# Optimization experiments

Hardware: AMD Instinct MI355X
Metric: run time of the kernel (lower is better)

## Reference

```python
import jax, jax.numpy as jnp
import numpy as np

B, S, D = 2, 2048, 1024
H, DK = 16, 64          # heads, d_k (= d_v)
DH = 4096               # FFN hidden
EPS = 1e-5


def _layer_norm(x, gamma, beta):
    mu = jnp.mean(x, axis=-1, keepdims=True)
    var = jnp.var(x, axis=-1, keepdims=True)
    return (x - mu) * jax.lax.rsqrt(var + EPS) * gamma + beta


def setup_inputs() -> dict:
    key = jax.random.key(0)
    ks = jax.random.split(key, 8)
    s = lambda fan_in: 1.0 / np.sqrt(fan_in)
    return {
        "x": jax.random.normal(ks[0], (B, S, D), dtype=jnp.float32),
        # NOTE: source module uses W_q for queries, keys AND values (bug kept faithfully),
        # so W_k / W_v are never used and are not materialized.
        "Wq": jax.random.normal(ks[1], (D, H * DK), dtype=jnp.float32) * s(D),
        "bq": jnp.zeros((H * DK,), dtype=jnp.float32),
        "Wo": jax.random.normal(ks[2], (H * DK, D), dtype=jnp.float32) * s(H * DK),
        "bo": jnp.zeros((D,), dtype=jnp.float32),
        "ln1_g": jnp.ones((D,), dtype=jnp.float32),
        "ln1_b": jnp.zeros((D,), dtype=jnp.float32),
        "W1": jax.random.normal(ks[3], (D, DH), dtype=jnp.float32) * s(D),
        "b1": jnp.zeros((DH,), dtype=jnp.float32),
        "W2": jax.random.normal(ks[4], (DH, D), dtype=jnp.float32) * s(DH),
        "b2": jnp.zeros((D,), dtype=jnp.float32),
        "ln2_g": jnp.ones((D,), dtype=jnp.float32),
        "ln2_b": jnp.zeros((D,), dtype=jnp.float32),
    }


def reference(x, Wq, bq, Wo, bo, ln1_g, ln1_b, W1, b1, W2, b2, ln2_g, ln2_b):
    residual = x
    # projections: q, k, v all use W_q (faithful to source)
    q = (x @ Wq + bq).reshape(B, S, H, DK)
    k = (x @ Wq + bq).reshape(B, S, H, DK)
    v = (x @ Wq + bq).reshape(B, S, H, DK)
    # scores scaled by sqrt(sequence_length), as in the source
    scale = 1.0 / jnp.sqrt(jnp.float32(S))
    scores = jnp.einsum("bqhd,bkhd->bhqk", q, k) * scale
    probs = jax.nn.softmax(scores, axis=-1)
    attn = jnp.einsum("bhqk,bkhd->bqhd", probs, v).reshape(B, S, H * DK)
    attn = attn @ Wo + bo
    # dropout is identity in eval mode
    x = _layer_norm(attn + residual, ln1_g, ln1_b)
    residual = x
    h = jax.nn.relu(x @ W1 + b1)
    x = h @ W2 + b2
    x = _layer_norm(x + residual, ln2_g, ln2_b)
    return x
```

## Files before the change

kernel.cpp:

```cpp
#include <hip/hip_runtime.h>
#include <stdint.h>


typedef unsigned short u16;
typedef __attribute__((ext_vector_type(8))) short v8s;
typedef __attribute__((ext_vector_type(4))) float v4f;

#define AS1 __attribute__((address_space(1)))
#define AS3 __attribute__((address_space(3)))

__device__ __forceinline__ void gl_lds16(const u16* g, u16* l) {
  __builtin_amdgcn_global_load_lds((const AS1 void*)g, (AS3 void*)l, 16, 0, 0);
}

__device__ __forceinline__ float bf2f(u16 u) {
  union { uint32_t i; float f; } v; v.i = ((uint32_t)u) << 16; return v.f;
}
__device__ __forceinline__ u16 f2bf(float f) {
  union { float f; uint32_t i; } v; v.f = f;
  uint32_t x = v.i;
  return (u16)((x + 0x7FFFu + ((x >> 16) & 1u)) >> 16);
}
__device__ __forceinline__ uint32_t fbits(float f) {
  union { float f; uint32_t u; } v; v.f = f; return v.u;
}

__global__ __launch_bounds__(256) void cvt_f2b(
    const float* __restrict__ src, u16* __restrict__ dst, int n4) {
  int i = (blockIdx.x * 256 + threadIdx.x);
  if (i < n4) {
    float4 v = *(const float4*)(src + (size_t)i * 4);
    ushort4 o;
    o.x = f2bf(v.x); o.y = f2bf(v.y); o.z = f2bf(v.z); o.w = f2bf(v.w);
    *(ushort4*)(dst + (size_t)i * 4) = o;
  }
}

__global__ __launch_bounds__(256) void transpose_f2b(
    const float* __restrict__ src, u16* __restrict__ dst,
    int R, int C, int ld_s, int ld_d) {
  __shared__ float tile[32][33];
  const int tx = threadIdx.x & 31, ty = threadIdx.x >> 5;
  const int c0 = blockIdx.x * 32, r0 = blockIdx.y * 32;
#pragma unroll
  for (int j = 0; j < 32; j += 8)
    tile[ty + j][tx] = src[(size_t)(r0 + ty + j) * ld_s + c0 + tx];
  __syncthreads();
#pragma unroll
  for (int j = 0; j < 32; j += 8)
    dst[(size_t)(c0 + ty + j) * ld_d + r0 + tx] = f2bf(tile[tx][ty + j]);
}

__global__ __launch_bounds__(256) void transpose_b2b(
    const u16* __restrict__ src, u16* __restrict__ dst,
    int R, int C, int ld_s, int ld_d) {
  __shared__ u16 tile[32][33];
  const int tx = threadIdx.x & 31, ty = threadIdx.x >> 5;
  const int c0 = blockIdx.x * 32, r0 = blockIdx.y * 32;
#pragma unroll
  for (int j = 0; j < 32; j += 8)
    tile[ty + j][tx] = src[(size_t)(r0 + ty + j) * ld_s + c0 + tx];
  __syncthreads();
#pragma unroll
  for (int j = 0; j < 32; j += 8)
    dst[(size_t)(c0 + ty + j) * ld_d + r0 + tx] = tile[tx][ty + j];
}

__global__ __launch_bounds__(512, 1) void gemm_8p(
    const u16* __restrict__ A, const u16* __restrict__ Bt,
    const float* __restrict__ bias, void* __restrict__ C0,
    u16* __restrict__ C1, u16* __restrict__ C2, u16* __restrict__ C3,
    int M, int N, int ldk, int klen, int relu, int c0_f32) {
  __shared__ u16 As[2][16384];
  __shared__ u16 Bs[2][16384];
  const int tid = threadIdx.x;
  const int w = tid >> 6, l = tid & 63;
  const int l16 = l & 15, kgrp = (l >> 4) & 3;
  const int wm = w >> 2, wn = w & 3;
  const int m0 = blockIdx.y * 256, n0 = blockIdx.x * 256;
  const int z = blockIdx.z;
  const int NT = klen >> 6;

  const int rl = tid >> 3;
  const int sw = 8 * ((tid & 7) ^ (rl & 7));
  const u16* gA[4]; const u16* gB[4];
#pragma unroll
  for (int j = 0; j < 4; j++) {
    gA[j] = A + (size_t)(m0 + j * 64 + rl) * ldk + (size_t)z * klen + sw;
    gB[j] = Bt + (size_t)(n0 + j * 64 + rl) * ldk + (size_t)z * klen + sw;
  }
  const int sdst = w * 512;

  const int ch0 = 8 * ((kgrp) ^ (l16 & 7));
  const int ch1 = 8 * ((4 + kgrp) ^ (l16 & 7));
  const int abase = (wm * 128 + l16) * 64;
  const int bbase = (wn * 64 + l16) * 64;

  v4f acc[8][4];
#pragma unroll
  for (int i = 0; i < 8; i++)
#pragma unroll
    for (int j = 0; j < 4; j++)
#pragma unroll
      for (int r = 0; r < 4; r++) acc[i][j][r] = 0.f;

  v8s a[4][2], b[4][2];

#define FENCE() asm volatile("" ::: "memory")
#define VMC(n) asm volatile("s_waitcnt vmcnt(" #n ")" ::: "memory")
#define BARX() { __builtin_amdgcn_s_barrier(); \
                 __builtin_amdgcn_sched_barrier(0); FENCE(); }
#define STGA(q, j, kt) gl_lds16(gA[j] + (size_t)(kt) * 64, &As[q][(j) * 4096 + sdst])
#define STGB(q, j, kt) gl_lds16(gB[j] + (size_t)(kt) * 64, &Bs[q][(j) * 4096 + sdst])
#define LDA(p, mh) { \
  const u16* Ap = &As[p][abase + (mh) * 4096]; \
  _Pragma("unroll") for (int mi = 0; mi < 4; mi++) { \
    a[mi][0] = *(const v8s*)(Ap + mi * 1024 + ch0); \
    a[mi][1] = *(const v8s*)(Ap + mi * 1024 + ch1); } }
#define LDB(p, nh) { \
  const u16* Bp = &Bs[p][bbase + (nh) * 2048]; \
  _Pragma("unroll") for (int ni = 0; ni < 2; ni++) { \
    b[(nh) * 2 + ni][0] = *(const v8s*)(Bp + ni * 1024 + ch0); \
    b[(nh) * 2 + ni][1] = *(const v8s*)(Bp + ni * 1024 + ch1); } }
#define MFQ(mh, nh) { \
  __builtin_amdgcn_s_setprio(1); \
  _Pragma("unroll") for (int ks = 0; ks < 2; ks++) \
  _Pragma("unroll") for (int mi = 0; mi < 4; mi++) \
  _Pragma("unroll") for (int ni = 0; ni < 2; ni++) \
    acc[(mh) * 4 + mi][(nh) * 2 + ni] = __builtin_amdgcn_mfma_f32_16x16x32_bf16( \
        a[mi][ks], b[(nh) * 2 + ni][ks], acc[(mh) * 4 + mi][(nh) * 2 + ni], 0, 0, 0); \
  __builtin_amdgcn_s_setprio(0); }

  STGA(0, 0, 0); STGA(0, 2, 0);
  FENCE();
  STGB(0, 0, 0); STGB(0, 1, 0);
  FENCE();
  STGB(0, 2, 0); STGB(0, 3, 0);
  FENCE();
  STGA(0, 1, 0); STGA(0, 3, 0);
  VMC(2); BARX();

  int p = 0;
  for (int kt = 0; kt < NT - 1; ++kt, p ^= 1) {
    const int q = p ^ 1;
    const int kn = kt + 1;
    LDA(p, 0);
    LDB(p, 0);
    FENCE();
    STGA(q, 0, kn); STGA(q, 2, kn);
    MFQ(0, 0);
    LDB(p, 1);
    FENCE();
    STGB(q, 0, kn); STGB(q, 1, kn);
    VMC(4); BARX();
    MFQ(0, 1);
    LDA(p, 1);
    FENCE();
    STGB(q, 2, kn); STGB(q, 3, kn);
    MFQ(1, 1);
    FENCE();
    STGA(q, 1, kn); STGA(q, 3, kn);
    VMC(2); BARX();
    MFQ(1, 0);
  }
  VMC(0); BARX();
  LDA(p, 0);
  LDB(p, 0);
  MFQ(0, 0);
  LDB(p, 1);
  MFQ(0, 1);
  LDA(p, 1);
  MFQ(1, 1);
  MFQ(1, 0);

#undef FENCE
#undef VMC
#undef BARX
#undef STGA
#undef STGB
#undef LDA
#undef LDB
#undef MFQ

#pragma unroll
  for (int mi = 0; mi < 8; mi++) {
    const int row = m0 + wm * 128 + mi * 16 + kgrp * 4;
#pragma unroll
    for (int ni = 0; ni < 4; ni++) {
      const int col = n0 + wn * 64 + ni * 16 + l16;
      float bv = (bias && z == 0) ? bias[col] : 0.f;
#pragma unroll
      for (int r = 0; r < 4; r++) {
        float v = acc[mi][ni][r] + bv;
        if (z == 0 && relu) v = fmaxf(v, 0.f);
        size_t idx = (size_t)(row + r) * N + col;
        if (z == 0) {
          if (c0_f32) ((float*)C0)[idx] = v;
          else ((u16*)C0)[idx] = f2bf(v);
        } else if (z == 1) {
          C1[idx] = f2bf(v);
        } else if (z == 2) {
          C2[idx] = f2bf(v);
        } else {
          C3[idx] = f2bf(v);
        }
      }
    }
  }
}

__global__ __launch_bounds__(256) void gemm_g2(
    const u16* __restrict__ A, const u16* __restrict__ Bt,
    const float* __restrict__ bias, void* __restrict__ C,
    int M, int N, int K, int relu, int accum, int out_f32) {
  __shared__ u16 As[2][8192];
  __shared__ u16 Bs[2][4096];
  const int tid = threadIdx.x;
  const int w = tid >> 6, l = tid & 63;
  const int l16 = l & 15, kgrp = l >> 4;
  const int m0 = blockIdx.y * 128, n0 = blockIdx.x * 64;
  const int wr = (w >> 1) * 64, wc = (w & 1) * 32;

  const int srow = w * 8 + (l >> 3);
  const u16* gA[4];
#pragma unroll
  for (int i = 0; i < 4; i++) {
    int r = i * 32 + srow;
    gA[i] = A + (size_t)(m0 + r) * K + 8 * ((l & 7) ^ (r & 7));
  }
  const u16* gB[2];
#pragma unroll
  for (int i = 0; i < 2; i++) {
    int r = i * 32 + srow;
    gB[i] = Bt + (size_t)(n0 + r) * K + 8 * ((l & 7) ^ (r & 7));
  }

  v4f acc[4][2];
#pragma unroll
  for (int i = 0; i < 4; i++)
#pragma unroll
    for (int j = 0; j < 2; j++)
#pragma unroll
      for (int r = 0; r < 4; r++) acc[i][j][r] = 0.f;

#pragma unroll
  for (int i = 0; i < 4; i++) gl_lds16(gA[i], &As[0][(i * 256 + w * 64) * 8]);
#pragma unroll
  for (int i = 0; i < 2; i++) gl_lds16(gB[i], &Bs[0][(i * 256 + w * 64) * 8]);

  int cur = 0;
  for (int k0 = 0; k0 < K; k0 += 64) {
    __syncthreads();
    if (k0 + 64 < K) {
      int nxt = cur ^ 1;
#pragma unroll
      for (int i = 0; i < 4; i++)
        gl_lds16(gA[i] + k0 + 64, &As[nxt][(i * 256 + w * 64) * 8]);
#pragma unroll
      for (int i = 0; i < 2; i++)
        gl_lds16(gB[i] + k0 + 64, &Bs[nxt][(i * 256 + w * 64) * 8]);
    }
    v8s a[4][2], b[2][2];
#pragma unroll
    for (int ks = 0; ks < 2; ks++) {
      int ch = 8 * ((ks * 4 + kgrp) ^ (l16 & 7));
#pragma unroll
      for (int mi = 0; mi < 4; mi++)
        a[mi][ks] = *(const v8s*)(&As[cur][(wr + mi * 16 + l16) * 64 + ch]);
#pragma unroll
      for (int ni = 0; ni < 2; ni++)
        b[ni][ks] = *(const v8s*)(&Bs[cur][(wc + ni * 16 + l16) * 64 + ch]);
    }
#pragma unroll
    for (int ks = 0; ks < 2; ks++)
#pragma unroll
      for (int mi = 0; mi < 4; mi++)
#pragma unroll
        for (int ni = 0; ni < 2; ni++)
          acc[mi][ni] = __builtin_amdgcn_mfma_f32_16x16x32_bf16(a[mi][ks], b[ni][ks], acc[mi][ni], 0, 0, 0);
    cur ^= 1;
  }

#pragma unroll
  for (int ni = 0; ni < 2; ni++) {
    int col = n0 + wc + ni * 16 + l16;
    float bv = bias ? bias[col] : 0.f;
#pragma unroll
    for (int mi = 0; mi < 4; mi++) {
      int row = m0 + wr + mi * 16 + kgrp * 4;
#pragma unroll
      for (int r = 0; r < 4; r++) {
        float v = acc[mi][ni][r] + bv;
        if (relu) v = fmaxf(v, 0.f);
        size_t idx = (size_t)(row + r) * N + col;
        if (out_f32) {
          float* Cf = (float*)C;
          if (accum) v += Cf[idx];
          Cf[idx] = v;
        } else {
          ((u16*)C)[idx] = f2bf(v);
        }
      }
    }
  }
}

__global__ __launch_bounds__(256) void attn_kernel(
    const u16* __restrict__ Q, const u16* __restrict__ Qt,
    u16* __restrict__ O) {
  __shared__ u16 KV[2][8192];
  __shared__ __align__(16) u16 Ps[4][2304];
  const int tid = threadIdx.x;
  const int w = tid >> 6, l = tid & 63;
  const int l16 = l & 15, kgrp = l >> 4;
  const int bh = blockIdx.y, b = bh >> 4, h = bh & 15;
  const int q0 = blockIdx.x * 128;
  const size_t rowQ = (size_t)(b * 2048 + q0 + w * 32);
  const float cexp = 1.4426950408889634f / 45.254833995939045f;

  const int srow = w * 8 + (l >> 3);
  const int sch8 = 8 * ((l & 7) ^ (srow & 7));
  const u16* gK0 = Q + (size_t)(b * 2048 + srow) * 1024 + h * 64 + sch8;
  const u16* gK1 = gK0 + (size_t)32 * 1024;
  const u16* gV0 = Qt + (size_t)(h * 64 + srow) * 4096 + b * 2048 + sch8;
  const u16* gV1 = gV0 + (size_t)32 * 4096;

  v8s qb[2][2];
#pragma unroll
  for (int nj = 0; nj < 2; nj++)
#pragma unroll
    for (int ks = 0; ks < 2; ks++) {
      v8s t = *(const v8s*)(Q + (rowQ + nj * 16 + l16) * 1024 + h * 64 + ks * 32 + kgrp * 8);
#pragma unroll
      for (int j = 0; j < 8; j++) t[j] = (short)f2bf(bf2f((u16)t[j]) * cexp);
      qb[nj][ks] = t;
    }

  v4f o[2][4];
  float ls[2] = {0.f, 0.f};
#pragma unroll
  for (int i = 0; i < 2; i++)
#pragma unroll
    for (int j = 0; j < 4; j++)
#pragma unroll
      for (int r = 0; r < 4; r++) o[i][j][r] = 0.f;

  gl_lds16(gK0, &KV[0][w * 512]);
  gl_lds16(gK1, &KV[0][2048 + w * 512]);
  gl_lds16(gV0, &KV[0][4096 + w * 512]);
  gl_lds16(gV1, &KV[0][4096 + 2048 + w * 512]);

  u16* Pw = &Ps[w][0];
  int cur = 0;
  for (int kb = 0; kb < 2048; kb += 64) {
    __syncthreads();
    if (kb + 64 < 2048) {
      int nxt = cur ^ 1;
      gl_lds16(gK0 + (size_t)(kb + 64) * 1024, &KV[nxt][w * 512]);
      gl_lds16(gK1 + (size_t)(kb + 64) * 1024, &KV[nxt][2048 + w * 512]);
      gl_lds16(gV0 + (kb + 64), &KV[nxt][4096 + w * 512]);
      gl_lds16(gV1 + (kb + 64), &KV[nxt][4096 + 2048 + w * 512]);
    }
    const u16* Ks = &KV[cur][0];
    const u16* Vt = &KV[cur][4096];

    v4f st[4][2];
#pragma unroll
    for (int i = 0; i < 4; i++)
#pragma unroll
      for (int j = 0; j < 2; j++)
#pragma unroll
        for (int r = 0; r < 4; r++) st[i][j][r] = 0.f;
#pragma unroll
    for (int ks = 0; ks < 2; ks++) {
      v8s ka[4];
#pragma unroll
      for (int mi = 0; mi < 4; mi++)
        ka[mi] = *(const v8s*)(Ks + (mi * 16 + l16) * 64 + 8 * ((ks * 4 + kgrp) ^ (l16 & 7)));
#pragma unroll
      for (int mi = 0; mi < 4; mi++)
#pragma unroll
        for (int nj = 0; nj < 2; nj++)
          st[mi][nj] = __builtin_amdgcn_mfma_f32_16x16x32_bf16(ka[mi], qb[nj][ks], st[mi][nj], 0, 0, 0);
    }

#pragma unroll
    for (int mi = 0; mi < 4; mi++)
#pragma unroll
      for (int nj = 0; nj < 2; nj++) {
        float p0 = __builtin_amdgcn_exp2f(st[mi][nj][0]);
        float p1 = __builtin_amdgcn_exp2f(st[mi][nj][1]);
        float p2 = __builtin_amdgcn_exp2f(st[mi][nj][2]);
        float p3 = __builtin_amdgcn_exp2f(st[mi][nj][3]);
        ls[nj] += (p0 + p1) + (p2 + p3);
        uint2 pk;
        pk.x = __builtin_amdgcn_perm(fbits(p1), fbits(p0), 0x07060302u);
        pk.y = __builtin_amdgcn_perm(fbits(p3), fbits(p2), 0x07060302u);
        *(uint2*)(Pw + (nj * 16 + l16) * 72 + mi * 16 + kgrp * 4) = pk;
      }

#pragma unroll
    for (int t = 0; t < 2; t++) {
      v8s pa[2], vb[4];
#pragma unroll
      for (int nj = 0; nj < 2; nj++)
        pa[nj] = *(const v8s*)(Pw + (nj * 16 + l16) * 72 + t * 32 + kgrp * 8);
#pragma unroll
      for (int ni = 0; ni < 4; ni++)
        vb[ni] = *(const v8s*)(Vt + (ni * 16 + l16) * 64 + 8 * ((t * 4 + kgrp) ^ (l16 & 7)));
#pragma unroll
      for (int nj = 0; nj < 2; nj++)
#pragma unroll
        for (int ni = 0; ni < 4; ni++)
          o[nj][ni] = __builtin_amdgcn_mfma_f32_16x16x32_bf16(pa[nj], vb[ni], o[nj][ni], 0, 0, 0);
    }
    cur ^= 1;
  }

#pragma unroll
  for (int nj = 0; nj < 2; nj++) {
    float t = ls[nj];
    t += __shfl_xor(t, 16, 64);
    t += __shfl_xor(t, 32, 64);
    ls[nj] = t;
  }

#pragma unroll
  for (int nj = 0; nj < 2; nj++) {
#pragma unroll
    for (int r = 0; r < 4; r++) {
      float den = __shfl(ls[nj], kgrp * 4 + r, 64);
      float rden = 1.f / den;
#pragma unroll
      for (int ni = 0; ni < 4; ni++) {
        O[(rowQ + nj * 16 + kgrp * 4 + r) * 1024 + h * 64 + ni * 16 + l16] =
            f2bf(o[nj][ni][r] * rden);
      }
    }
  }
}

__global__ __launch_bounds__(256) void ln_residual(
    const void* __restrict__ Y, const void* __restrict__ Y2,
    const void* __restrict__ Y3, const void* __restrict__ Y4,
    const void* __restrict__ Xr,
    const float* __restrict__ g, const float* __restrict__ bb,
    void* __restrict__ out, int yf, int y2f, int xf, int of) {
  const int row = blockIdx.x, tid = threadIdx.x;
  const size_t base = (size_t)row * 1024;
  float v[4], s = 0.f, sq = 0.f;
#pragma unroll
  for (int i = 0; i < 4; i++) {
    int c = tid + i * 256;
    float ya = yf ? ((const float*)Y)[base + c] : bf2f(((const u16*)Y)[base + c]);
    float xa = xf ? ((const float*)Xr)[base + c] : bf2f(((const u16*)Xr)[base + c]);
    float x = ya + xa;
    if (Y2) {
      float y2a = y2f ? ((const float*)Y2)[base + c] : bf2f(((const u16*)Y2)[base + c]);
      x += y2a;
    }
    if (Y3) x += bf2f(((const u16*)Y3)[base + c]);
    if (Y4) x += bf2f(((const u16*)Y4)[base + c]);
    v[i] = x; s += x; sq += x * x;
  }
#pragma unroll
  for (int off = 32; off >= 1; off >>= 1) {
    s += __shfl_down(s, off, 64);
    sq += __shfl_down(sq, off, 64);
  }
  __shared__ float rs[4], rq[4];
  const int w = tid >> 6, l = tid & 63;
  if (l == 0) { rs[w] = s; rq[w] = sq; }
  __syncthreads();
  s = rs[0] + rs[1] + rs[2] + rs[3];
  sq = rq[0] + rq[1] + rq[2] + rq[3];
  const float mu = s * (1.f / 1024.f);
  const float var = sq * (1.f / 1024.f) - mu * mu;
  const float rstd = rsqrtf(var + 1e-5f);
#pragma unroll
  for (int i = 0; i < 4; i++) {
    int c = tid + i * 256;
    float r = (v[i] - mu) * rstd * g[c] + bb[c];
    if (of) ((float*)out)[base + c] = r;
    else ((u16*)out)[base + c] = f2bf(r);
  }
}

extern "C" void kernel_launch(void* const* d_in, const int* in_sizes, int n_in,
                              void* d_out, int out_size, void* d_ws, size_t ws_size,
                              hipStream_t stream) {
  const float* x   = (const float*)d_in[0];
  const float* Wq  = (const float*)d_in[1];
  const float* bq  = (const float*)d_in[2];
  const float* Wo  = (const float*)d_in[3];
  const float* bo  = (const float*)d_in[4];
  const float* g1  = (const float*)d_in[5];
  const float* be1 = (const float*)d_in[6];
  const float* W1  = (const float*)d_in[7];
  const float* b1  = (const float*)d_in[8];
  const float* W2  = (const float*)d_in[9];
  const float* b2  = (const float*)d_in[10];
  const float* g2  = (const float*)d_in[11];
  const float* be2 = (const float*)d_in[12];
  float* out = (float*)d_out;
  u16* ws  = (u16*)d_ws;

  const size_t M1 = 1048576;
  dim3 blk(256);
  dim3 blk8(512);
  const bool big = ws_size >= (size_t)37 * M1 * 2;

  if (big) {
    u16* xb   = ws + 0;
    u16* Qb   = ws + 4 * M1;
    u16* Qt   = ws + 8 * M1;
    u16* WqT  = ws + 12 * M1;
    u16* W1T  = ws + 13 * M1;
    u16* W2T  = ws + 17 * M1;
    u16* Hh   = ws + 21 * M1;
    u16* attn = xb;  u16* Yb = Qt;  u16* x1 = Qb;  u16* WoT = WqT;
    u16* P1wo = W1T;
    u16* P2wo = W2T;
    u16* P3wo = Hh;
    u16* P1f2 = Qt;
    u16* P2f2 = xb;
    u16* P3f2 = W1T;

    cvt_f2b<<<dim3(4096), blk, 0, stream>>>(x, xb, 1048576);
    transpose_f2b<<<dim3(32, 32), blk, 0, stream>>>(Wq, WqT, 1024, 1024, 1024, 1024);
    gemm_g2<<<dim3(16, 32), blk, 0, stream>>>(xb, WqT, bq, Qb, 4096, 1024, 1024, 0, 0, 0);

    transpose_b2b<<<dim3(32, 128), blk, 0, stream>>>(Qb, Qt, 4096, 1024, 1024, 4096);
    attn_kernel<<<dim3(16, 32), blk, 0, stream>>>(Qb, Qt, attn);

    transpose_f2b<<<dim3(32, 32), blk, 0, stream>>>(Wo, WoT, 1024, 1024, 1024, 1024);
    gemm_8p<<<dim3(4, 16, 4), blk8, 0, stream>>>(attn, WoT, bo, Yb, P1wo, P2wo, P3wo,
                                                 4096, 1024, 1024, 256, 0, 0);
    ln_residual<<<dim3(4096), blk, 0, stream>>>(Yb, P1wo, P2wo, P3wo, x, g1, be1, x1,
                                                0, 0, 1, 0);

    transpose_f2b<<<dim3(128, 32), blk, 0, stream>>>(W1, W1T, 1024, 4096, 4096, 1024);
    gemm_8p<<<dim3(16, 16, 1), blk8, 0, stream>>>(x1, W1T, b1, Hh,
                                                  nullptr, nullptr, nullptr,
                                                  4096, 4096, 1024, 1024, 1, 0);

    transpose_f2b<<<dim3(32, 128), blk, 0, stream>>>(W2, W2T, 4096, 1024, 1024, 4096);
    gemm_8p<<<dim3(4, 16, 4), blk8, 0, stream>>>(Hh, W2T, b2, out, P1f2, P2f2, P3f2,
                                                 4096, 1024, 4096, 1024, 0, 1);

    ln_residual<<<dim3(4096), blk, 0, stream>>>(out, P1f2, P2f2, P3f2, x1, g2, be2, out,
                                                1, 0, 0, 1);
  } else {
    u16* xb   = ws + 0;
    u16* Qb   = ws + 4 * M1;
    u16* Qt   = ws + 8 * M1;
    u16* attn = xb;  u16* Yb = Qt;  u16* x1 = Qb;  u16* Hc = xb;
    u16* Wt1  = ws + 12 * M1;
    u16* Wt2  = ws + 13 * M1;

    cvt_f2b<<<dim3(4096), blk, 0, stream>>>(x, xb, 1048576);
    transpose_f2b<<<dim3(32, 32), blk, 0, stream>>>(Wq, Wt1, 1024, 1024, 1024, 1024);
    gemm_g2<<<dim3(16, 32), blk, 0, stream>>>(xb, Wt1, bq, Qb, 4096, 1024, 1024, 0, 0, 0);

    transpose_b2b<<<dim3(32, 128), blk, 0, stream>>>(Qb, Qt, 4096, 1024, 1024, 4096);
    attn_kernel<<<dim3(16, 32), blk, 0, stream>>>(Qb, Qt, attn);

    transpose_f2b<<<dim3(32, 32), blk, 0, stream>>>(Wo, Wt2, 1024, 1024, 1024, 1024);
    gemm_g2<<<dim3(16, 32), blk, 0, stream>>>(attn, Wt2, bo, Yb, 4096, 1024, 1024, 0, 0, 0);
    ln_residual<<<dim3(4096), blk, 0, stream>>>(Yb, nullptr, nullptr, nullptr, x, g1, be1,
                                                x1, 0, 0, 1, 0);

    for (int c = 0; c < 4; c++) {
      transpose_f2b<<<dim3(32, 32), blk, 0, stream>>>(W1 + (size_t)c * 1024, Wt1,
                                                      1024, 1024, 4096, 1024);
      gemm_g2<<<dim3(16, 32), blk, 0, stream>>>(x1, Wt1, b1 + (size_t)c * 1024, Hc,
                                                4096, 1024, 1024, 1, 0, 0);
      transpose_f2b<<<dim3(32, 32), blk, 0, stream>>>(W2 + (size_t)c * M1, Wt2,
                                                      1024, 1024, 1024, 1024);
      gemm_g2<<<dim3(16, 32), blk, 0, stream>>>(Hc, Wt2, (c == 0) ? b2 : (const float*)nullptr,
                                                out, 4096, 1024, 1024, 0, (c > 0) ? 1 : 0, 1);
    }
    ln_residual<<<dim3(4096), blk, 0, stream>>>(out, nullptr, nullptr, nullptr, x1, g2, be2,
                                                out, 1, 0, 0, 1);
  }
}
```

Measured before the change: 347.6 us.

## Split attention block across 8 waves with 16 query rows each

The attention kernel now launches 512 threads per block instead of 256. Each of 8 waves handles 16 query rows instead of 32, and the K/V tile loading is split so four waves load K and four load V. The aim is more waves in flight to hide latency and lower per-wave register pressure. In exchange, each K/V tile loaded into LDS is reused by fewer query rows per wave, and the block is larger, which may limit occupancy.

```diff
diff --git a/kernel.cpp b/kernel.cpp
--- a/kernel.cpp
+++ b/kernel.cpp
@@ -305,50 +305,52 @@
   }
 }
 
-__global__ __launch_bounds__(256) void attn_kernel(
+__global__ __launch_bounds__(512) void attn_kernel(
     const u16* __restrict__ Q, const u16* __restrict__ Qt,
     u16* __restrict__ O) {
   __shared__ u16 KV[2][8192];
-  __shared__ __align__(16) u16 Ps[4][2304];
+  __shared__ __align__(16) u16 Ps[8][1152];
   const int tid = threadIdx.x;
   const int w = tid >> 6, l = tid & 63;
   const int l16 = l & 15, kgrp = l >> 4;
   const int bh = blockIdx.y, b = bh >> 4, h = bh & 15;
   const int q0 = blockIdx.x * 128;
-  const size_t rowQ = (size_t)(b * 2048 + q0 + w * 32);
+  const size_t rowQ = (size_t)(b * 2048 + q0 + w * 16);
   const float cexp = 1.4426950408889634f / 45.254833995939045f;
 
-  const int srow = w * 8 + (l >> 3);
-  const int sch8 = 8 * ((l & 7) ^ (srow & 7));
-  const u16* gK0 = Q + (size_t)(b * 2048 + srow) * 1024 + h * 64 + sch8;
-  const u16* gK1 = gK0 + (size_t)32 * 1024;
-  const u16* gV0 = Qt + (size_t)(h * 64 + srow) * 4096 + b * 2048 + sch8;
-  const u16* gV1 = gV0 + (size_t)32 * 4096;
-
-  v8s qb[2][2];
-#pragma unroll
-  for (int nj = 0; nj < 2; nj++)
-#pragma unroll
-    for (int ks = 0; ks < 2; ks++) {
-      v8s t = *(const v8s*)(Q + (rowQ + nj * 16 + l16) * 1024 + h * 64 + ks * 32 + kgrp * 8);
-#pragma unroll
-      for (int j = 0; j < 8; j++) t[j] = (short)f2bf(bf2f((u16)t[j]) * cexp);
-      qb[nj][ks] = t;
-    }
-
-  v4f o[2][4];
-  float ls[2] = {0.f, 0.f};
-#pragma unroll
-  for (int i = 0; i < 2; i++)
-#pragma unroll
-    for (int j = 0; j < 4; j++)
-#pragma unroll
-      for (int r = 0; r < 4; r++) o[i][j][r] = 0.f;
-
-  gl_lds16(gK0, &KV[0][w * 512]);
-  gl_lds16(gK1, &KV[0][2048 + w * 512]);
-  gl_lds16(gV0, &KV[0][4096 + w * 512]);
-  gl_lds16(gV1, &KV[0][4096 + 2048 + w * 512]);
+  const int isV = w >> 2, wl = w & 3;
+  const int r0 = wl * 16 + (l >> 3);
+  const int sch8 = 8 * ((l & 7) ^ (l >> 3));
+  const u16* gS0;
+  size_t kstep;
+  if (!isV) {
+    gS0 = Q + (size_t)(b * 2048 + r0) * 1024 + h * 64 + sch8;
+    kstep = 1024;
+  } else {
+    gS0 = Qt + (size_t)(h * 64 + r0) * 4096 + b * 2048 + sch8;
+    kstep = 1;
+  }
+  const u16* gS1 = gS0 + (size_t)8 * (isV ? 4096 : 1024);
+  const int ldst = isV * 4096 + wl * 1024;
+
+  v8s qb[2];
+#pragma unroll
+  for (int ks = 0; ks < 2; ks++) {
+    v8s t = *(const v8s*)(Q + (rowQ + l16) * 1024 + h * 64 + ks * 32 + kgrp * 8);
+#pragma unroll
+    for (int j = 0; j < 8; j++) t[j] = (short)f2bf(bf2f((u16)t[j]) * cexp);
+    qb[ks] = t;
+  }
+
+  v4f o[4];
+  float ls = 0.f;
+#pragma unroll
+  for (int j = 0; j < 4; j++)
+#pragma unroll
+    for (int r = 0; r < 4; r++) o[j][r] = 0.f;
+
+  gl_lds16(gS0, &KV[0][ldst]);
+  gl_lds16(gS1, &KV[0][ldst + 512]);
 
   u16* Pw = &Ps[w][0];
   int cur = 0;
@@ -356,21 +358,17 @@
     __syncthreads();
     if (kb + 64 < 2048) {
       int nxt = cur ^ 1;
-      gl_lds16(gK0 + (size_t)(kb + 64) * 1024, &KV[nxt][w * 512]);
-      gl_lds16(gK1 + (size_t)(kb + 64) * 1024, &KV[nxt][2048 + w * 512]);
-      gl_lds16(gV0 + (kb + 64), &KV[nxt][4096 + w * 512]);
-      gl_lds16(gV1 + (kb + 64), &KV[nxt][4096 + 2048 + w * 512]);
+      gl_lds16(gS0 + (size_t)(kb + 64) * kstep, &KV[nxt][ldst]);
+      gl_lds16(gS1 + (size_t)(kb + 64) * kstep, &KV[nxt][ldst + 512]);
     }
     const u16* Ks = &KV[cur][0];
     const u16* Vt = &KV[cur][4096];
 
-    v4f st[4][2];
+    v4f st[4];
 #pragma unroll
     for (int i = 0; i < 4; i++)
 #pragma unroll
-      for (int j = 0; j < 2; j++)
-#pragma unroll
-        for (int r = 0; r < 4; r++) st[i][j][r] = 0.f;
+      for (int r = 0; r < 4; r++) st[i][r] = 0.f;
 #pragma unroll
     for (int ks = 0; ks < 2; ks++) {
       v8s ka[4];
@@ -379,63 +377,51 @@
         ka[mi] = *(const v8s*)(Ks + (mi * 16 + l16) * 64 + 8 * ((ks * 4 + kgrp) ^ (l16 & 7)));
 #pragma unroll
       for (int mi = 0; mi < 4; mi++)
-#pragma unroll
-        for (int nj = 0; nj < 2; nj++)
-          st[mi][nj] = __builtin_amdgcn_mfma_f32_16x16x32_bf16(ka[mi], qb[nj][ks], st[mi][nj], 0, 0, 0);
-    }
-
-#pragma unroll
-    for (int mi = 0; mi < 4; mi++)
-#pragma unroll
-      for (int nj = 0; nj < 2; nj++) {
-        float p0 = __builtin_amdgcn_exp2f(st[mi][nj][0]);
-        float p1 = __builtin_amdgcn_exp2f(st[mi][nj][1]);
-        float p2 = __builtin_amdgcn_exp2f(st[mi][nj][2]);
-        float p3 = __builtin_amdgcn_exp2f(st[mi][nj][3]);
-        ls[nj] += (p0 + p1) + (p2 + p3);
-        uint2 pk;
-        pk.x = __builtin_amdgcn_perm(fbits(p1), fbits(p0), 0x07060302u);
-        pk.y = __builtin_amdgcn_perm(fbits(p3), fbits(p2), 0x07060302u);
-        *(uint2*)(Pw + (nj * 16 + l16) * 72 + mi * 16 + kgrp * 4) = pk;
-      }
+        st[mi] = __builtin_amdgcn_mfma_f32_16x16x32_bf16(ka[mi], qb[ks], st[mi], 0, 0, 0);
+    }
+
+#pragma unroll
+    for (int mi = 0; mi < 4; mi++) {
+      float p0 = __builtin_amdgcn_exp2f(st[mi][0]);
+      float p1 = __builtin_amdgcn_exp2f(st[mi][1]);
+      float p2 = __builtin_amdgcn_exp2f(st[mi][2]);
+      float p3 = __builtin_amdgcn_exp2f(st[mi][3]);
+      ls += (p0 + p1) + (p2 + p3);
+      uint2 pk;
+      pk.x = __builtin_amdgcn_perm(fbits(p1), fbits(p0), 0x07060302u);
+      pk.y = __builtin_amdgcn_perm(fbits(p3), fbits(p2), 0x07060302u);
+      *(uint2*)(Pw + l16 * 72 + mi * 16 + kgrp * 4) = pk;
+    }
 
 #pragma unroll
     for (int t = 0; t < 2; t++) {
-      v8s pa[2], vb[4];
-#pragma unroll
-      for (int nj = 0; nj < 2; nj++)
-        pa[nj] = *(const v8s*)(Pw + (nj * 16 + l16) * 72 + t * 32 + kgrp * 8);
+      v8s pa, vb[4];
+      pa = *(const v8s*)(Pw + l16 * 72 + t * 32 + kgrp * 8);
 #pragma unroll
       for (int ni = 0; ni < 4; ni++)
         vb[ni] = *(const v8s*)(Vt + (ni * 16 + l16) * 64 + 8 * ((t * 4 + kgrp) ^ (l16 & 7)));
 #pragma unroll
-      for (int nj = 0; nj < 2; nj++)
-#pragma unroll
-        for (int ni = 0; ni < 4; ni++)
-          o[nj][ni] = __builtin_amdgcn_mfma_f32_16x16x32_bf16(pa[nj], vb[ni], o[nj][ni], 0, 0, 0);
+      for (int ni = 0; ni < 4; ni++)
+        o[ni] = __builtin_amdgcn_mfma_f32_16x16x32_bf16(pa, vb[ni], o[ni], 0, 0, 0);
     }
     cur ^= 1;
   }
 
-#pragma unroll
-  for (int nj = 0; nj < 2; nj++) {
-    float t = ls[nj];
+  {
+    float t = ls;
     t += __shfl_xor(t, 16, 64);
     t += __shfl_xor(t, 32, 64);
-    ls[nj] = t;
-  }
-
-#pragma unroll
-  for (int nj = 0; nj < 2; nj++) {
-#pragma unroll
-    for (int r = 0; r < 4; r++) {
-      float den = __shfl(ls[nj], kgrp * 4 + r, 64);
-      float rden = 1.f / den;
-#pragma unroll
-      for (int ni = 0; ni < 4; ni++) {
-        O[(rowQ + nj * 16 + kgrp * 4 + r) * 1024 + h * 64 + ni * 16 + l16] =
-            f2bf(o[nj][ni][r] * rden);
-      }
+    ls = t;
+  }
+
+#pragma unroll
+  for (int r = 0; r < 4; r++) {
+    float den = __shfl(ls, kgrp * 4 + r, 64);
+    float rden = 1.f / den;
+#pragma unroll
+    for (int ni = 0; ni < 4; ni++) {
+      O[(rowQ + kgrp * 4 + r) * 1024 + h * 64 + ni * 16 + l16] =
+          f2bf(o[ni][r] * rden);
     }
   }
 }
@@ -531,7 +517,7 @@
     gemm_g2<<<dim3(16, 32), blk, 0, stream>>>(xb, WqT, bq, Qb, 4096, 1024, 1024, 0, 0, 0);
 
     transpose_b2b<<<dim3(32, 128), blk, 0, stream>>>(Qb, Qt, 4096, 1024, 1024, 4096);
-    attn_kernel<<<dim3(16, 32), blk, 0, stream>>>(Qb, Qt, attn);
+    attn_kernel<<<dim3(16, 32), blk8, 0, stream>>>(Qb, Qt, attn);
 
     transpose_f2b<<<dim3(32, 32), blk, 0, stream>>>(Wo, WoT, 1024, 1024, 1024, 1024);
     gemm_8p<<<dim3(4, 16, 4), blk8, 0, stream>>>(attn, WoT, bo, Yb, P1wo, P2wo, P3wo,
@@ -563,7 +549,7 @@
     gemm_g2<<<dim3(16, 32), blk, 0, stream>>>(xb, Wt1, bq, Qb, 4096, 1024, 1024, 0, 0, 0);
 
     transpose_b2b<<<dim3(32, 128), blk, 0, stream>>>(Qb, Qt, 4096, 1024, 1024, 4096);
-    attn_kernel<<<dim3(16, 32), blk, 0, stream>>>(Qb, Qt, attn);
+    attn_kernel<<<dim3(16, 32), blk8, 0, stream>>>(Qb, Qt, attn);
 
     transpose_f2b<<<dim3(32, 32), blk, 0, stream>>>(Wo, Wt2, 1024, 1024, 1024, 1024);
     gemm_g2<<<dim3(16, 32), blk, 0, stream>>>(attn, Wt2, bo, Yb, 4096, 1024, 1024, 0, 0, 0);
```

Measured after the change: 341.7 us. Within noise of the previous version (-1.7%).
